# Performance work log

Measured on AMD Instinct MI355X. Metric: run time of the kernel, lower is better.

Reference implementation:

```python
import jax, jax.numpy as jnp
import numpy as np

HEADS = 8
SR = 2
EPS_BN = 1e-5
EPS_LN = 1e-5


def _conv(x, w, b, stride=1, pad=0):
    y = jax.lax.conv_general_dilated(x, w, (stride, stride), [(pad, pad), (pad, pad)],
                                     dimension_numbers=('NCHW', 'OIHW', 'NCHW'))
    return y + b[None, :, None, None]


def _bn(x, g, b):
    # eval-mode BatchNorm with running_mean=0, running_var=1
    return x * (g / jnp.sqrt(1.0 + EPS_BN))[None, :, None, None] + b[None, :, None, None]


def _dwt_haar(x):
    # [B,c,H,W] -> [B,4c,H/2,W/2] stacked as LL,HL,LH,HH (Wave-ViT convention)
    x1 = x[:, :, 0::2, 0::2] / 2
    x2 = x[:, :, 1::2, 0::2] / 2
    x3 = x[:, :, 0::2, 1::2] / 2
    x4 = x[:, :, 1::2, 1::2] / 2
    ll = x1 + x2 + x3 + x4
    hl = -x1 - x2 + x3 + x4
    lh = -x1 + x2 - x3 + x4
    hh = x1 - x2 - x3 + x4
    return jnp.concatenate([ll, hl, lh, hh], axis=1)


def _idwt_haar(y):
    # [B,4c,h,w] -> [B,c,2h,2w], exact inverse of _dwt_haar
    c = y.shape[1] // 4
    ll, hl, lh, hh = y[:, :c], y[:, c:2 * c], y[:, 2 * c:3 * c], y[:, 3 * c:]
    p1 = (ll - hl - lh + hh) / 2  # (0::2, 0::2)
    p2 = (ll - hl + lh - hh) / 2  # (1::2, 0::2)
    p3 = (ll + hl - lh - hh) / 2  # (0::2, 1::2)
    p4 = (ll + hl + lh + hh) / 2  # (1::2, 1::2)
    B, _, h2, w2 = ll.shape
    row0 = jnp.stack([p1, p3], axis=-1)  # even rows
    row1 = jnp.stack([p2, p4], axis=-1)  # odd rows
    out = jnp.stack([row0, row1], axis=3)  # [B,c,h2,2,w2,2]
    return out.reshape(B, c, 2 * h2, 2 * w2)


def setup_inputs() -> dict:
    key = jax.random.key(0)
    ks = jax.random.split(key, 12)
    B, H, W, C = 8, 56, 56, 512
    N = H * W
    c4 = C // 4

    def nrm(k, shp, std):
        return jax.random.normal(k, shp, jnp.float32) * std

    return {
        'x': jax.random.normal(ks[0], (B, N, C), jnp.float32),
        'H': H, 'W': W,
        'reduce_w': nrm(ks[1], (c4, C, 1, 1), (2.0 / c4) ** 0.5),
        'reduce_b': jnp.zeros((c4,), jnp.float32),
        'reduce_g': jnp.ones((c4,), jnp.float32),
        'reduce_beta': jnp.zeros((c4,), jnp.float32),
        'filter_w': nrm(ks[2], (C, C, 3, 3), (2.0 / (9 * C)) ** 0.5),
        'filter_b': jnp.zeros((C,), jnp.float32),
        'filter_g': jnp.ones((C,), jnp.float32),
        'filter_beta': jnp.zeros((C,), jnp.float32),
        'q_w': nrm(ks[3], (C, C), 0.02),
        'q_b': jnp.zeros((C,), jnp.float32),
        'ln_g': jnp.ones((C,), jnp.float32),
        'ln_b': jnp.zeros((C,), jnp.float32),
        'kv_w': nrm(ks[4], (2 * C, C), 0.02),
        'kv_b': jnp.zeros((2 * C,), jnp.float32),
        'kve_w': nrm(ks[5], (C, C, SR, SR), (2.0 / (SR * SR * C)) ** 0.5),
        'kve_b': jnp.zeros((C,), jnp.float32),
        'proj_w': nrm(ks[6], (C, C + c4), 0.02),
        'proj_b': jnp.zeros((C,), jnp.float32),
    }


def reference(x, H, W, reduce_w, reduce_b, reduce_g, reduce_beta,
              filter_w, filter_b, filter_g, filter_beta,
              q_w, q_b, ln_g, ln_b, kv_w, kv_b, kve_w, kve_b, proj_w, proj_b):
    B, N, C = x.shape
    hd = C // HEADS
    scale = hd ** -0.5

    q = (x @ q_w.T + q_b).reshape(B, N, HEADS, hd).transpose(0, 2, 1, 3)  # [B,h,N,d]

    xi = x.reshape(B, H, W, C).transpose(0, 3, 1, 2)  # NCHW
    r = jax.nn.relu(_bn(_conv(xi, reduce_w, reduce_b), reduce_g, reduce_beta))  # [B,C/4,H,W]
    r16 = r.astype(jnp.float16)
    x_dwt = _dwt_haar(r16).astype(jnp.float32)  # [B,C,H/2,W/2]
    x_dwt = jax.nn.relu(_bn(_conv(x_dwt, filter_w, filter_b, pad=1), filter_g, filter_beta))
    x_dwt16 = x_dwt.astype(jnp.float16)
    x_idwt = _idwt_haar(x_dwt16)  # [B,C/4,H,W] fp16
    x_idwt = x_idwt.reshape(B, C // 4, H * W).transpose(0, 2, 1)  # [B,N,C/4]

    x_dwt = x_dwt16.astype(jnp.float32)
    kv_in = _conv(x_dwt, kve_w, kve_b, stride=SR).reshape(B, C, -1).transpose(0, 2, 1)  # [B,M,C]
    mu = kv_in.mean(-1, keepdims=True)
    var = ((kv_in - mu) ** 2).mean(-1, keepdims=True)
    kv_n = (kv_in - mu) / jnp.sqrt(var + EPS_LN) * ln_g + ln_b
    kv = (kv_n @ kv_w.T + kv_b).reshape(B, -1, 2, HEADS, hd).transpose(2, 0, 3, 1, 4)
    k, v = kv[0], kv[1]  # [B,h,M,d]

    attn = jax.nn.softmax(jnp.einsum('bhnd,bhmd->bhnm', q, k) * scale, axis=-1)
    o = jnp.einsum('bhnm,bhmd->bhnd', attn, v).transpose(0, 2, 1, 3).reshape(B, N, C)
    o = jnp.concatenate([o, x_idwt.astype(jnp.float32)], axis=-1)  # [B,N,C+C/4]
    return o @ proj_w.T + proj_b
```

## Files before the change

kernel.cpp:

```cpp
#include <hip/hip_runtime.h>
#include <math.h>


typedef _Float16 half8 __attribute__((ext_vector_type(8)));
typedef _Float16 half4v __attribute__((ext_vector_type(4)));
typedef float f32x4 __attribute__((ext_vector_type(4)));

static const size_t OFF_X16  = 0;
static const size_t OFF_Q16  = 12845056;
static const size_t OFF_CAT  = 25690112;
static const size_t OFF_R16  = 41746432;
static const size_t OFF_PAD  = 44957696;
static const size_t OFF_DWTB = 48644096;
static const size_t OFF_KVIN = 51855360;
static const size_t OFF_LN16 = 55066624;
static const size_t OFF_KV16 = 55869440;
static const size_t OFF_WT   = 57475072;
static const size_t OFF_KT   = 59834368;
static const size_t OFF_QW   = 60882944;
static const size_t OFF_KVW  = 61145088;
static const size_t OFF_PW   = 61669376;
static const size_t OFF_RW   = 61997056;
static const size_t OFF_VT   = 62062592;
static const size_t OFF_PART = 62980096;

#define BN_RSQ 0.9999950000374997f
#define SCL2   0.1803368801111204f
#define PART_STRIDE 3211264
#define KVE_STRIDE  802816

__device__ __forceinline__ void async_copy16(const _Float16* g, _Float16* l) {
    __builtin_amdgcn_global_load_lds(
        (const __attribute__((address_space(1))) void*)g,
        (__attribute__((address_space(3))) void*)l, 16, 0, 0);
}

#define WAIT4_BARRIER() asm volatile("s_waitcnt vmcnt(4)\n\ts_barrier" ::: "memory")
#define WAIT0_BARRIER() asm volatile("s_waitcnt vmcnt(0)\n\ts_barrier" ::: "memory")

template <int ALOAD, int EPI>
__global__ __launch_bounds__(256) void gemm16(
    const _Float16* __restrict__ A, const _Float16* __restrict__ W,
    void* __restrict__ outp, int M, int K, int lda, int ldc,
    const float* __restrict__ bias, const float* __restrict__ bng,
    const float* __restrict__ bnb)
{
    __shared__ _Float16 sA[3][128 * 32];
    __shared__ _Float16 sB[3][128 * 32];
    const int t = threadIdx.x;
    const int lane = t & 63, wid = t >> 6;

    int bx = blockIdx.x, by = blockIdx.y;
    {
        int nwg = gridDim.x * gridDim.y;
        if ((nwg & 7) == 0) {
            int orig = by * gridDim.x + bx;
            int cs = nwg >> 3;
            int wg = (orig & 7) * cs + (orig >> 3);
            by = wg % gridDim.y;
            bx = wg / gridDim.y;
        }
    }
    const int m0 = bx * 128, n0 = by * 128;
    const int kbase = blockIdx.z * K;

    const int sr = wid * 16 + (lane >> 2);
    const int sc = (lane & 3) * 8;
    const int stA0 = wid * 512;
    const int stA1 = 2048 + wid * 512;

    const _Float16 *aP0, *aP1;
    if constexpr (ALOAD == 0) {
        int r0 = m0 + sr;      if (r0 > M - 1) r0 = M - 1;
        int r1 = m0 + 64 + sr; if (r1 > M - 1) r1 = M - 1;
        aP0 = A + (size_t)r0 * lda + sc;
        aP1 = A + (size_t)r1 * lda + sc;
    } else {
        int m_ = m0 + sr; if (m_ > M - 1) m_ = M - 1;
        int b_ = m_ / 196, rem = m_ - b_ * 196, i_ = rem / 14, j_ = rem - i_ * 14;
        aP0 = A + ((size_t)(b_ * 784 + 2 * i_ * 28 + 2 * j_)) * 512 + sc;
        m_ = m0 + 64 + sr; if (m_ > M - 1) m_ = M - 1;
        b_ = m_ / 196; rem = m_ - b_ * 196; i_ = rem / 14; j_ = rem - i_ * 14;
        aP1 = A + ((size_t)(b_ * 784 + 2 * i_ * 28 + 2 * j_)) * 512 + sc;
    }
    const int ldw = (ALOAD == 2) ? lda : K;
    const _Float16* bP0 = W + (size_t)(n0 + sr) * ldw + sc;
    const _Float16* bP1 = W + (size_t)(n0 + 64 + sr) * ldw + sc;

    const int mw = wid & 1, nw = wid >> 1;
    const int pAoff = (mw * 64 + (lane & 15)) * 32 + (lane >> 4) * 8;
    const int pBoff = (nw * 64 + (lane & 15)) * 32 + (lane >> 4) * 8;

    f32x4 acc[4][4];
#pragma unroll
    for (int i = 0; i < 4; ++i)
#pragma unroll
        for (int j = 0; j < 4; ++j) acc[i][j] = (f32x4)(0.0f);

    auto aoff_of = [&](int k) -> int {
        if constexpr (ALOAD == 0) {
            return k;
        } else {
            int sub = k >> 9; int ky = sub >> 1, kx = sub & 1;
            return (ky * 28 + kx) * 512 + (k & 511);
        }
    };
    auto stage = [&](int ti, int buf) {
        int k = kbase + ti * 32;
        int aOff = aoff_of(k);
        async_copy16(aP0 + aOff, &sA[buf][stA0]);
        async_copy16(aP1 + aOff, &sA[buf][stA1]);
        async_copy16(bP0 + k, &sB[buf][stA0]);
        async_copy16(bP1 + k, &sB[buf][stA1]);
    };

    const int nt = K >> 5;
    stage(0, 0);
    if (nt > 1) { stage(1, 1); WAIT4_BARRIER(); }
    else        { WAIT0_BARRIER(); }

    int cur = 0;
    for (int i = 0; i < nt; ++i) {
        const _Float16* pA = &sA[cur][0] + pAoff;
        const _Float16* pB = &sB[cur][0] + pBoff;
        half8 aF[4], bF[4];
#pragma unroll
        for (int u = 0; u < 4; ++u) aF[u] = *(const half8*)(pA + u * 512);
#pragma unroll
        for (int u = 0; u < 4; ++u) bF[u] = *(const half8*)(pB + u * 512);

        const bool st = (i + 2 < nt);
        if (st) {
            int nb = cur + 2; if (nb >= 3) nb -= 3;
            stage(i + 2, nb);
        }
#pragma unroll
        for (int u = 0; u < 4; ++u)
#pragma unroll
            for (int j = 0; j < 4; ++j)
                acc[u][j] = __builtin_amdgcn_mfma_f32_16x16x32_f16(
                    aF[u], bF[j], acc[u][j], 0, 0, 0);

        if (i + 1 < nt) {
            if (st) WAIT4_BARRIER();
            else    WAIT0_BARRIER();
        }
        ++cur; if (cur == 3) cur = 0;
    }

    const int orow = m0 + mw * 64 + (lane >> 4) * 4;
    const int ocol = n0 + nw * 64 + (lane & 15);
#pragma unroll
    for (int j = 0; j < 4; ++j) {
        int col = ocol + j * 16;
        float bv = 0.0f, g = 0.0f, b2 = 0.0f;
        if constexpr (EPI != 3) bv = bias[col];
        if constexpr (EPI == 1) { g = bng[col] * BN_RSQ; b2 = bnb[col]; }
#pragma unroll
        for (int i = 0; i < 4; ++i) {
#pragma unroll
            for (int r = 0; r < 4; ++r) {
                int row = orow + i * 16 + r;
                if (row >= M) continue;
                float v = acc[i][j][r] + bv;
                if constexpr (EPI == 1) v = fmaxf(v * g + b2, 0.0f);
                if constexpr (EPI == 0)
                    ((float*)outp)[(size_t)row * ldc + col] = v;
                else if constexpr (EPI == 3)
                    ((float*)outp)[(size_t)blockIdx.z * KVE_STRIDE
                                   + (size_t)row * ldc + col] = v;
                else
                    ((_Float16*)outp)[(size_t)row * ldc + col] = (_Float16)v;
            }
        }
    }
}

__global__ __launch_bounds__(256) void conv_splitk(
    const _Float16* __restrict__ A, const _Float16* __restrict__ W,
    float* __restrict__ partA, float* __restrict__ partB)
{
    __shared__ _Float16 sA[3][128 * 32];
    __shared__ _Float16 sB[3][128 * 32];
    const int t = threadIdx.x;
    const int lane = t & 63, wid = t >> 6;

    int orig = blockIdx.x;
    int wg = (orig & 7) * 98 + (orig >> 3);
    int bx = wg % 49;  int c = wg / 49;
    int by = c & 3,    bz = c >> 2;

    const int m0 = bx * 128, n0 = by * 128;
    const int kbase = bz * 1152;

    const int sr = wid * 16 + (lane >> 2);
    const int sc = (lane & 3) * 8;
    const int stA0 = wid * 512;
    const int stA1 = 2048 + wid * 512;

    int m_ = m0 + sr;
    int b_ = m_ / 784, rem = m_ - b_ * 784, y_ = rem / 28, x_ = rem - y_ * 28;
    const _Float16* aP0 = A + ((size_t)(b_ * 900 + (y_ + 1) * 30 + (x_ + 1))) * 512 + sc;
    m_ = m0 + 64 + sr;
    b_ = m_ / 784; rem = m_ - b_ * 784; y_ = rem / 28; x_ = rem - y_ * 28;
    const _Float16* aP1 = A + ((size_t)(b_ * 900 + (y_ + 1) * 30 + (x_ + 1))) * 512 + sc;
    const _Float16* bP0 = W + (size_t)(n0 + sr) * 4608 + sc;
    const _Float16* bP1 = W + (size_t)(n0 + 64 + sr) * 4608 + sc;

    const int mw = wid & 1, nw = wid >> 1;
    const int pAoff = (mw * 64 + (lane & 15)) * 32 + (lane >> 4) * 8;
    const int pBoff = (nw * 64 + (lane & 15)) * 32 + (lane >> 4) * 8;

    f32x4 acc[4][4];
#pragma unroll
    for (int i = 0; i < 4; ++i)
#pragma unroll
        for (int j = 0; j < 4; ++j) acc[i][j] = (f32x4)(0.0f);

    auto aoff_of = [&](int k) -> int {
        int sub = k >> 9; int s3 = sub / 3;
        int dy = s3 - 1, dx = sub - s3 * 3 - 1;
        return (dy * 30 + dx) * 512 + (k & 511);
    };
    auto stage = [&](int ti, int buf) {
        int k = kbase + ti * 32;
        int aOff = aoff_of(k);
        async_copy16(aP0 + aOff, &sA[buf][stA0]);
        async_copy16(aP1 + aOff, &sA[buf][stA1]);
        async_copy16(bP0 + k, &sB[buf][stA0]);
        async_copy16(bP1 + k, &sB[buf][stA1]);
    };

    const int nt = 36;
    stage(0, 0);
    stage(1, 1);
    WAIT4_BARRIER();

    int cur = 0;
    for (int i = 0; i < nt; ++i) {
        const _Float16* pA = &sA[cur][0] + pAoff;
        const _Float16* pB = &sB[cur][0] + pBoff;
        half8 aF[4], bF[4];
#pragma unroll
        for (int u = 0; u < 4; ++u) aF[u] = *(const half8*)(pA + u * 512);
#pragma unroll
        for (int u = 0; u < 4; ++u) bF[u] = *(const half8*)(pB + u * 512);

        const bool st = (i + 2 < nt);
        if (st) {
            int nb = cur + 2; if (nb >= 3) nb -= 3;
            stage(i + 2, nb);
        }
#pragma unroll
        for (int u = 0; u < 4; ++u)
#pragma unroll
            for (int j = 0; j < 4; ++j)
                acc[u][j] = __builtin_amdgcn_mfma_f32_16x16x32_f16(
                    aF[u], bF[j], acc[u][j], 0, 0, 0);

        if (i + 1 < nt) {
            if (st) WAIT4_BARRIER();
            else    WAIT0_BARRIER();
        }
        ++cur; if (cur == 3) cur = 0;
    }

    float* dst = (bz < 2) ? (partA + (size_t)bz * PART_STRIDE)
                          : (partB + (size_t)(bz - 2) * PART_STRIDE);
    const int orow = m0 + mw * 64 + (lane >> 4) * 4;
    const int ocol = n0 + nw * 64 + (lane & 15);
#pragma unroll
    for (int j = 0; j < 4; ++j) {
#pragma unroll
        for (int i = 0; i < 4; ++i)
#pragma unroll
            for (int r = 0; r < 4; ++r)
                dst[(size_t)(orow + i * 16 + r) * 512 + ocol + j * 16] = acc[i][j][r];
    }
}

__global__ __launch_bounds__(256) void conv_epi(
    const float* __restrict__ pA, const float* __restrict__ pB,
    _Float16* __restrict__ o, const float* __restrict__ bias,
    const float* __restrict__ bng, const float* __restrict__ bnb)
{
    int i = blockIdx.x * 256 + threadIdx.x;
    size_t base = (size_t)i * 8;
    int c = (int)(base & 511);
    half8 hv;
#pragma unroll
    for (int u = 0; u < 8; u += 4) {
        float4 a0 = *(const float4*)(pA + base + u);
        float4 a1 = *(const float4*)(pA + PART_STRIDE + base + u);
        float4 a2 = *(const float4*)(pB + base + u);
        float4 a3 = *(const float4*)(pB + PART_STRIDE + base + u);
        float s[4] = {a0.x + a1.x + a2.x + a3.x, a0.y + a1.y + a2.y + a3.y,
                      a0.z + a1.z + a2.z + a3.z, a0.w + a1.w + a2.w + a3.w};
#pragma unroll
        for (int v = 0; v < 4; ++v) {
            int cc = c + u + v;
            float val = (s[v] + bias[cc]) * (bng[cc] * BN_RSQ) + bnb[cc];
            hv[u + v] = (_Float16)fmaxf(val, 0.0f);
        }
    }
    *(half8*)(o + base) = hv;
}

__global__ __launch_bounds__(256) void cvt_f32_f16(
    const float* __restrict__ s, _Float16* __restrict__ d, int n8)
{
    int i = blockIdx.x * 256 + threadIdx.x;
    if (i >= n8) return;
    const float4* sp = (const float4*)(s + (size_t)i * 8);
    float4 a = sp[0], b = sp[1];
    half8 h;
    h[0] = (_Float16)a.x; h[1] = (_Float16)a.y; h[2] = (_Float16)a.z; h[3] = (_Float16)a.w;
    h[4] = (_Float16)b.x; h[5] = (_Float16)b.y; h[6] = (_Float16)b.z; h[7] = (_Float16)b.w;
    *(half8*)(d + (size_t)i * 8) = h;
}

__global__ __launch_bounds__(256) void zero_half(_Float16* __restrict__ p, int n8)
{
    int i = blockIdx.x * 256 + threadIdx.x;
    if (i < n8) *(float4*)(p + (size_t)i * 8) = make_float4(0.f, 0.f, 0.f, 0.f);
}

__global__ __launch_bounds__(256) void transpose_filter16(
    const float* __restrict__ fw, _Float16* __restrict__ wT)
{
    int idx = blockIdx.x * 256 + threadIdx.x;
    int n = idx / 4608; int r = idx - n * 4608;
    int sub = r >> 9; int ci = r & 511;
    wT[idx] = (_Float16)fw[(size_t)n * 4608 + ci * 9 + sub];
}

__global__ __launch_bounds__(256) void transpose_kve16(
    const float* __restrict__ kw, _Float16* __restrict__ kT)
{
    int idx = blockIdx.x * 256 + threadIdx.x;
    int n = idx >> 11; int r = idx & 2047;
    int sub = r >> 9; int ci = r & 511;
    kT[idx] = (_Float16)kw[((size_t)n << 11) + (ci << 2) + sub];
}

__global__ __launch_bounds__(256) void vt_prep(
    const _Float16* __restrict__ kv, _Float16* __restrict__ vt)
{
    int idx = blockIdx.x * 256 + threadIdx.x;
    int m = idx % 224;
    int rest = idx / 224;
    int d = rest & 63;
    int bh = rest >> 6;
    int b = bh >> 3, h = bh & 7;
    _Float16 v = (_Float16)0.0f;
    if (m < 196)
        v = kv[((size_t)(b * 196 + m)) * 1024 + 512 + h * 64 + d];
    vt[idx] = v;
}

__global__ __launch_bounds__(128) void dwt_kernel(
    const _Float16* __restrict__ r, _Float16* __restrict__ pad)
{
    int bid = blockIdx.x;
    int b = bid / 784; int rem = bid - b * 784;
    int i = rem / 28;  int j = rem - i * 28;
    int c = threadIdx.x;
    int y = 2 * i, x = 2 * j;
    size_t base = (size_t)b * 3136;
    _Float16 f1 = r[(base + (size_t)y * 56 + x) * 128 + c];
    _Float16 f2 = r[(base + (size_t)(y + 1) * 56 + x) * 128 + c];
    _Float16 f3 = r[(base + (size_t)y * 56 + (x + 1)) * 128 + c];
    _Float16 f4 = r[(base + (size_t)(y + 1) * 56 + (x + 1)) * 128 + c];
    _Float16 h = (_Float16)0.5f;
    _Float16 x1 = f1 * h, x2 = f2 * h, x3 = f3 * h, x4 = f4 * h;
    _Float16 ll = ((x1 + x2) + x3) + x4;
    _Float16 hl = (((-x1) - x2) + x3) + x4;
    _Float16 lh = (((-x1) + x2) - x3) + x4;
    _Float16 hh = ((x1 - x2) - x3) + x4;
    size_t ob = ((size_t)b * 900 + (size_t)(i + 1) * 30 + (j + 1)) * 512;
    pad[ob + c]       = ll;
    pad[ob + 128 + c] = hl;
    pad[ob + 256 + c] = lh;
    pad[ob + 384 + c] = hh;
}

__global__ __launch_bounds__(128) void idwt_kernel(
    const _Float16* __restrict__ d, _Float16* __restrict__ cat)
{
    int bid = blockIdx.x;
    int b = bid / 784; int rem = bid - b * 784;
    int i = rem / 28;  int j = rem - i * 28;
    int c = threadIdx.x;
    size_t ib = ((size_t)b * 784 + (size_t)i * 28 + j) * 512;
    _Float16 ll = d[ib + c];
    _Float16 hl = d[ib + 128 + c];
    _Float16 lh = d[ib + 256 + c];
    _Float16 hh = d[ib + 384 + c];
    _Float16 h = (_Float16)0.5f;
    _Float16 p1 = (((ll - hl) - lh) + hh) * h;
    _Float16 p2 = (((ll - hl) + lh) - hh) * h;
    _Float16 p3 = (((ll + hl) - lh) - hh) * h;
    _Float16 p4 = (((ll + hl) + lh) + hh) * h;
    int y = 2 * i, x = 2 * j;
    size_t rb = (size_t)b * 3136;
    cat[(rb + (size_t)y * 56 + x) * 640 + 512 + c]           = p1;
    cat[(rb + (size_t)y * 56 + x + 1) * 640 + 512 + c]       = p3;
    cat[(rb + (size_t)(y + 1) * 56 + x) * 640 + 512 + c]     = p2;
    cat[(rb + (size_t)(y + 1) * 56 + x + 1) * 640 + 512 + c] = p4;
}

__global__ __launch_bounds__(256) void ln_kernel(
    const float* __restrict__ part, _Float16* __restrict__ o,
    const float* __restrict__ g, const float* __restrict__ bta,
    const float* __restrict__ kvb)
{
    int wave = threadIdx.x >> 6;
    int lane = threadIdx.x & 63;
    int row = blockIdx.x * 4 + wave;
    int c = lane * 8;
    const float* rp = part + (size_t)row * 512 + c;
    float v[8];
#pragma unroll
    for (int i = 0; i < 8; i += 4) {
        float4 a0 = *(const float4*)(rp + i);
        float4 a1 = *(const float4*)(rp + KVE_STRIDE + i);
        float4 a2 = *(const float4*)(rp + 2 * KVE_STRIDE + i);
        float4 a3 = *(const float4*)(rp + 3 * KVE_STRIDE + i);
        v[i + 0] = (a0.x + a1.x) + (a2.x + a3.x) + kvb[c + i + 0];
        v[i + 1] = (a0.y + a1.y) + (a2.y + a3.y) + kvb[c + i + 1];
        v[i + 2] = (a0.z + a1.z) + (a2.z + a3.z) + kvb[c + i + 2];
        v[i + 3] = (a0.w + a1.w) + (a2.w + a3.w) + kvb[c + i + 3];
    }
    float s = ((v[0] + v[1]) + (v[2] + v[3])) + ((v[4] + v[5]) + (v[6] + v[7]));
#pragma unroll
    for (int off = 32; off; off >>= 1) s += __shfl_xor(s, off);
    float mu = s * (1.0f / 512.0f);
    float sq = 0.0f;
#pragma unroll
    for (int i = 0; i < 8; ++i) { v[i] -= mu; sq += v[i] * v[i]; }
#pragma unroll
    for (int off = 32; off; off >>= 1) sq += __shfl_xor(sq, off);
    float inv = 1.0f / sqrtf(sq * (1.0f / 512.0f) + 1e-5f);
    half8 hv;
#pragma unroll
    for (int i = 0; i < 8; ++i) hv[i] = (_Float16)(v[i] * inv * g[c + i] + bta[c + i]);
    *(half8*)(o + (size_t)row * 512 + c) = hv;
}

__global__ __launch_bounds__(256) void attn_mfma(
    const _Float16* __restrict__ q, const _Float16* __restrict__ kv,
    const _Float16* __restrict__ vt, _Float16* __restrict__ cat)
{
    __shared__ _Float16 sK[64][72];
    __shared__ _Float16 sVT[64][72];
    __shared__ _Float16 sP[4][16][40];
    int bid = blockIdx.x;
    int qt = bid % 49;
    int h  = (bid / 49) & 7;
    int b  = bid / 392;
    int n0 = qt * 64;
    int t = threadIdx.x, lane = t & 63, wid = t >> 6;
    int quad = lane >> 4, l16 = lane & 15;

    const _Float16* qp = q + ((size_t)(b * 3136 + n0 + wid * 16 + l16)) * 512
                           + h * 64 + quad * 8;
    half8 aQ0 = *(const half8*)qp;
    half8 aQ1 = *(const half8*)(qp + 32);

    f32x4 oacc[4];
#pragma unroll
    for (int i = 0; i < 4; ++i) oacc[i] = (f32x4)(0.0f);
    float lsum[4] = {0.f, 0.f, 0.f, 0.f};

    const _Float16* vtb = vt + ((size_t)((b * 8 + h) * 64)) * 224;

    for (int c0 = 0; c0 < 224; c0 += 64) {
        __syncthreads();
#pragma unroll
        for (int it = 0; it < 2; ++it) {
            int slot = t + 256 * it;
            int row = slot >> 3, c8 = (slot & 7) * 8;
            int m = c0 + row; if (m > 195) m = 195;
            *(half8*)&sK[row][c8] =
                *(const half8*)(kv + ((size_t)(b * 196 + m)) * 1024 + h * 64 + c8);
        }
#pragma unroll
        for (int it = 0; it < 2; ++it) {
            int slot = t + 256 * it;
            int row = slot >> 3, c8 = (slot & 7) * 8;
            *(half8*)&sVT[row][c8] =
                *(const half8*)(vtb + (size_t)row * 224 + c0 + c8);
        }
        __syncthreads();

#pragma unroll
        for (int sc = 0; sc < 64; sc += 32) {
            half8 bk00 = *(const half8*)&sK[sc + l16][quad * 8];
            half8 bk01 = *(const half8*)&sK[sc + l16][32 + quad * 8];
            half8 bk10 = *(const half8*)&sK[sc + 16 + l16][quad * 8];
            half8 bk11 = *(const half8*)&sK[sc + 16 + l16][32 + quad * 8];
            f32x4 s0 = (f32x4)(0.0f), s1 = (f32x4)(0.0f);
            s0 = __builtin_amdgcn_mfma_f32_16x16x32_f16(aQ0, bk00, s0, 0, 0, 0);
            s0 = __builtin_amdgcn_mfma_f32_16x16x32_f16(aQ1, bk01, s0, 0, 0, 0);
            s1 = __builtin_amdgcn_mfma_f32_16x16x32_f16(aQ0, bk10, s1, 0, 0, 0);
            s1 = __builtin_amdgcn_mfma_f32_16x16x32_f16(aQ1, bk11, s1, 0, 0, 0);

            int col0 = c0 + sc + l16;
            float msk0 = (col0 < 196) ? 0.0f : -INFINITY;
            float msk1 = (col0 + 16 < 196) ? 0.0f : -INFINITY;
            float p0[4], p1[4];
#pragma unroll
            for (int r = 0; r < 4; ++r) {
                p0[r] = exp2f(s0[r] * SCL2 + msk0);
                p1[r] = exp2f(s1[r] * SCL2 + msk1);
                lsum[r] += p0[r] + p1[r];
            }
#pragma unroll
            for (int r = 0; r < 4; ++r) {
                sP[wid][quad * 4 + r][l16]      = (_Float16)p0[r];
                sP[wid][quad * 4 + r][16 + l16] = (_Float16)p1[r];
            }
            half8 aP = *(const half8*)&sP[wid][l16][quad * 8];
            half8 bv0 = *(const half8*)&sVT[l16][sc + quad * 8];
            half8 bv1 = *(const half8*)&sVT[16 + l16][sc + quad * 8];
            half8 bv2 = *(const half8*)&sVT[32 + l16][sc + quad * 8];
            half8 bv3 = *(const half8*)&sVT[48 + l16][sc + quad * 8];
            oacc[0] = __builtin_amdgcn_mfma_f32_16x16x32_f16(aP, bv0, oacc[0], 0, 0, 0);
            oacc[1] = __builtin_amdgcn_mfma_f32_16x16x32_f16(aP, bv1, oacc[1], 0, 0, 0);
            oacc[2] = __builtin_amdgcn_mfma_f32_16x16x32_f16(aP, bv2, oacc[2], 0, 0, 0);
            oacc[3] = __builtin_amdgcn_mfma_f32_16x16x32_f16(aP, bv3, oacc[3], 0, 0, 0);
        }
    }

    float inv[4];
#pragma unroll
    for (int r = 0; r < 4; ++r) {
        float s = lsum[r];
        s += __shfl_xor(s, 1);
        s += __shfl_xor(s, 2);
        s += __shfl_xor(s, 4);
        s += __shfl_xor(s, 8);
        inv[r] = 1.0f / s;
    }
#pragma unroll
    for (int r = 0; r < 4; ++r) {
        size_t rowoff = ((size_t)(b * 3136 + n0 + wid * 16 + quad * 4 + r)) * 640
                        + h * 64 + l16;
#pragma unroll
        for (int tv = 0; tv < 4; ++tv)
            cat[rowoff + tv * 16] = (_Float16)(oacc[tv][r] * inv[r]);
    }
}

extern "C" void kernel_launch(void* const* d_in, const int* in_sizes, int n_in,
                              void* d_out, int out_size, void* d_ws, size_t ws_size,
                              hipStream_t stream)
{
    const float* x           = (const float*)d_in[0];
    const float* reduce_w    = (const float*)d_in[3];
    const float* reduce_b    = (const float*)d_in[4];
    const float* reduce_g    = (const float*)d_in[5];
    const float* reduce_beta = (const float*)d_in[6];
    const float* filter_w    = (const float*)d_in[7];
    const float* filter_b    = (const float*)d_in[8];
    const float* filter_g    = (const float*)d_in[9];
    const float* filter_beta = (const float*)d_in[10];
    const float* q_w         = (const float*)d_in[11];
    const float* q_b         = (const float*)d_in[12];
    const float* ln_g        = (const float*)d_in[13];
    const float* ln_b        = (const float*)d_in[14];
    const float* kv_w        = (const float*)d_in[15];
    const float* kv_b        = (const float*)d_in[16];
    const float* kve_w       = (const float*)d_in[17];
    const float* kve_b       = (const float*)d_in[18];
    const float* proj_w      = (const float*)d_in[19];
    const float* proj_b      = (const float*)d_in[20];
    float* out = (float*)d_out;
    _Float16* hws = (_Float16*)d_ws;

    _Float16* x16    = hws + OFF_X16;
    _Float16* q16    = hws + OFF_Q16;
    _Float16* cat16  = hws + OFF_CAT;
    _Float16* r16    = hws + OFF_R16;
    _Float16* pad16  = hws + OFF_PAD;
    _Float16* dwtb16 = hws + OFF_DWTB;
    _Float16* ln16   = hws + OFF_LN16;
    _Float16* kv16   = hws + OFF_KV16;
    _Float16* wT16   = hws + OFF_WT;
    _Float16* kT16   = hws + OFF_KT;
    _Float16* qw16   = hws + OFF_QW;
    _Float16* kvw16  = hws + OFF_KVW;
    _Float16* pw16   = hws + OFF_PW;
    _Float16* rw16   = hws + OFF_RW;
    _Float16* vt16   = hws + OFF_VT;
    float*    partA  = (float*)(hws + OFF_X16);
    float*    partB  = (float*)(hws + OFF_PART);
    float*    kvepart = (float*)(hws + OFF_X16);

    cvt_f32_f16<<<dim3(6272), dim3(256), 0, stream>>>(x, x16, 1605632);
    cvt_f32_f16<<<dim3(128),  dim3(256), 0, stream>>>(q_w, qw16, 32768);
    cvt_f32_f16<<<dim3(256),  dim3(256), 0, stream>>>(kv_w, kvw16, 65536);
    cvt_f32_f16<<<dim3(160),  dim3(256), 0, stream>>>(proj_w, pw16, 40960);
    cvt_f32_f16<<<dim3(32),   dim3(256), 0, stream>>>(reduce_w, rw16, 8192);
    transpose_filter16<<<dim3(9216), dim3(256), 0, stream>>>(filter_w, wT16);
    transpose_kve16<<<dim3(4096), dim3(256), 0, stream>>>(kve_w, kT16);
    zero_half<<<dim3(1800), dim3(256), 0, stream>>>(pad16, 460800);

    gemm16<0, 2><<<dim3(196, 4), dim3(256), 0, stream>>>(
        x16, qw16, q16, 25088, 512, 512, 512, q_b, nullptr, nullptr);

    gemm16<0, 1><<<dim3(196, 1), dim3(256), 0, stream>>>(
        x16, rw16, r16, 25088, 512, 512, 128, reduce_b, reduce_g, reduce_beta);

    dwt_kernel<<<dim3(6272), dim3(128), 0, stream>>>(r16, pad16);

    conv_splitk<<<dim3(784), dim3(256), 0, stream>>>(pad16, wT16, partA, partB);
    conv_epi<<<dim3(1568), dim3(256), 0, stream>>>(
        partA, partB, dwtb16, filter_b, filter_g, filter_beta);

    idwt_kernel<<<dim3(6272), dim3(128), 0, stream>>>(dwtb16, cat16);

    gemm16<2, 3><<<dim3(13, 4, 4), dim3(256), 0, stream>>>(
        dwtb16, kT16, kvepart, 1568, 512, 2048, 512, nullptr, nullptr, nullptr);

    ln_kernel<<<dim3(392), dim3(256), 0, stream>>>(kvepart, ln16, ln_g, ln_b, kve_b);

    gemm16<0, 2><<<dim3(13, 8), dim3(256), 0, stream>>>(
        ln16, kvw16, kv16, 1568, 512, 512, 1024, kv_b, nullptr, nullptr);

    vt_prep<<<dim3(3584), dim3(256), 0, stream>>>(kv16, vt16);

    attn_mfma<<<dim3(3136), dim3(256), 0, stream>>>(q16, kv16, vt16, cat16);

    gemm16<0, 0><<<dim3(196, 4), dim3(256), 0, stream>>>(
        cat16, pw16, out, 25088, 640, 640, 512, proj_b, nullptr, nullptr);
}
```

Baseline: 421.5 us.

## Fuse q and reduce GEMMs into one launch and use nontemporal stores

The q projection and the 1x1 reduce conv both read x16, so their weights are now concatenated into one buffer and computed by a single GEMM launch with 5 column tiles. A new epilogue mode routes the last tile through bias+BN+ReLU into r16 and the others into q16. Separately, streaming outputs (fp32 GEMM outputs, split-K partials, cat writes) use nontemporal stores, and conv_epi reads its partials with nontemporal loads, to reduce cache pollution. This saves one launch and one pass over x16, at the cost of a per-tile branch in the epilogue.

```diff
diff --git a/kernel.cpp b/kernel.cpp
--- a/kernel.cpp
+++ b/kernel.cpp
@@ -12,7 +12,7 @@
 static const size_t OFF_R16  = 41746432;
 static const size_t OFF_PAD  = 44957696;
 static const size_t OFF_DWTB = 48644096;
-static const size_t OFF_KVIN = 51855360;
+static const size_t OFF_QRW  = 51855360;
 static const size_t OFF_LN16 = 55066624;
 static const size_t OFF_KV16 = 55869440;
 static const size_t OFF_WT   = 57475072;
@@ -43,7 +43,8 @@
     const _Float16* __restrict__ A, const _Float16* __restrict__ W,
     void* __restrict__ outp, int M, int K, int lda, int ldc,
     const float* __restrict__ bias, const float* __restrict__ bng,
-    const float* __restrict__ bnb)
+    const float* __restrict__ bnb, const float* __restrict__ bias2,
+    void* __restrict__ outp2)
 {
     __shared__ _Float16 sA[3][128 * 32];
     __shared__ _Float16 sB[3][128 * 32];
@@ -154,7 +155,17 @@
     for (int j = 0; j < 4; ++j) {
         int col = ocol + j * 16;
         float bv = 0.0f, g = 0.0f, b2 = 0.0f;
-        if constexpr (EPI != 3) bv = bias[col];
+        if constexpr (EPI == 4) {
+            if (n0 >= 512) {
+                bv = bias2[col - 512];
+                g = bng[col - 512] * BN_RSQ;
+                b2 = bnb[col - 512];
+            } else {
+                bv = bias[col];
+            }
+        } else if constexpr (EPI != 3) {
+            bv = bias[col];
+        }
         if constexpr (EPI == 1) { g = bng[col] * BN_RSQ; b2 = bnb[col]; }
 #pragma unroll
         for (int i = 0; i < 4; ++i) {
@@ -164,13 +175,24 @@
                 if (row >= M) continue;
                 float v = acc[i][j][r] + bv;
                 if constexpr (EPI == 1) v = fmaxf(v * g + b2, 0.0f);
-                if constexpr (EPI == 0)
-                    ((float*)outp)[(size_t)row * ldc + col] = v;
-                else if constexpr (EPI == 3)
-                    ((float*)outp)[(size_t)blockIdx.z * KVE_STRIDE
-                                   + (size_t)row * ldc + col] = v;
-                else
+                if constexpr (EPI == 0) {
+                    __builtin_nontemporal_store(
+                        v, (float*)outp + (size_t)row * ldc + col);
+                } else if constexpr (EPI == 3) {
+                    __builtin_nontemporal_store(
+                        v, (float*)outp + (size_t)blockIdx.z * KVE_STRIDE
+                           + (size_t)row * ldc + col);
+                } else if constexpr (EPI == 4) {
+                    if (n0 >= 512) {
+                        v = fmaxf(v * g + b2, 0.0f);
+                        ((_Float16*)outp2)[(size_t)row * 128 + (col - 512)] =
+                            (_Float16)v;
+                    } else {
+                        ((_Float16*)outp)[(size_t)row * ldc + col] = (_Float16)v;
+                    }
+                } else {
                     ((_Float16*)outp)[(size_t)row * ldc + col] = (_Float16)v;
+                }
             }
         }
     }
@@ -275,7 +297,9 @@
         for (int i = 0; i < 4; ++i)
 #pragma unroll
             for (int r = 0; r < 4; ++r)
-                dst[(size_t)(orow + i * 16 + r) * 512 + ocol + j * 16] = acc[i][j][r];
+                __builtin_nontemporal_store(
+                    acc[i][j][r],
+                    &dst[(size_t)(orow + i * 16 + r) * 512 + ocol + j * 16]);
     }
 }
 
@@ -290,16 +314,15 @@
     half8 hv;
 #pragma unroll
     for (int u = 0; u < 8; u += 4) {
-        float4 a0 = *(const float4*)(pA + base + u);
-        float4 a1 = *(const float4*)(pA + PART_STRIDE + base + u);
-        float4 a2 = *(const float4*)(pB + base + u);
-        float4 a3 = *(const float4*)(pB + PART_STRIDE + base + u);
-        float s[4] = {a0.x + a1.x + a2.x + a3.x, a0.y + a1.y + a2.y + a3.y,
-                      a0.z + a1.z + a2.z + a3.z, a0.w + a1.w + a2.w + a3.w};
+        f32x4 a0 = __builtin_nontemporal_load((const f32x4*)(pA + base + u));
+        f32x4 a1 = __builtin_nontemporal_load((const f32x4*)(pA + PART_STRIDE + base + u));
+        f32x4 a2 = __builtin_nontemporal_load((const f32x4*)(pB + base + u));
+        f32x4 a3 = __builtin_nontemporal_load((const f32x4*)(pB + PART_STRIDE + base + u));
 #pragma unroll
         for (int v = 0; v < 4; ++v) {
             int cc = c + u + v;
-            float val = (s[v] + bias[cc]) * (bng[cc] * BN_RSQ) + bnb[cc];
+            float s = (a0[v] + a1[v]) + (a2[v] + a3[v]);
+            float val = (s + bias[cc]) * (bng[cc] * BN_RSQ) + bnb[cc];
             hv[u + v] = (_Float16)fmaxf(val, 0.0f);
         }
     }
@@ -403,10 +426,10 @@
     _Float16 p4 = (((ll + hl) + lh) + hh) * h;
     int y = 2 * i, x = 2 * j;
     size_t rb = (size_t)b * 3136;
-    cat[(rb + (size_t)y * 56 + x) * 640 + 512 + c]           = p1;
-    cat[(rb + (size_t)y * 56 + x + 1) * 640 + 512 + c]       = p3;
-    cat[(rb + (size_t)(y + 1) * 56 + x) * 640 + 512 + c]     = p2;
-    cat[(rb + (size_t)(y + 1) * 56 + x + 1) * 640 + 512 + c] = p4;
+    __builtin_nontemporal_store(p1, &cat[(rb + (size_t)y * 56 + x) * 640 + 512 + c]);
+    __builtin_nontemporal_store(p3, &cat[(rb + (size_t)y * 56 + x + 1) * 640 + 512 + c]);
+    __builtin_nontemporal_store(p2, &cat[(rb + (size_t)(y + 1) * 56 + x) * 640 + 512 + c]);
+    __builtin_nontemporal_store(p4, &cat[(rb + (size_t)(y + 1) * 56 + x + 1) * 640 + 512 + c]);
 }
 
 __global__ __launch_bounds__(256) void ln_kernel(
@@ -548,7 +571,8 @@
                         + h * 64 + l16;
 #pragma unroll
         for (int tv = 0; tv < 4; ++tv)
-            cat[rowoff + tv * 16] = (_Float16)(oacc[tv][r] * inv[r]);
+            __builtin_nontemporal_store(
+                (_Float16)(oacc[tv][r] * inv[r]), &cat[rowoff + tv * 16]);
     }
 }
 
@@ -584,33 +608,30 @@
     _Float16* r16    = hws + OFF_R16;
     _Float16* pad16  = hws + OFF_PAD;
     _Float16* dwtb16 = hws + OFF_DWTB;
+    _Float16* qrw16  = hws + OFF_QRW;
     _Float16* ln16   = hws + OFF_LN16;
     _Float16* kv16   = hws + OFF_KV16;
     _Float16* wT16   = hws + OFF_WT;
     _Float16* kT16   = hws + OFF_KT;
-    _Float16* qw16   = hws + OFF_QW;
     _Float16* kvw16  = hws + OFF_KVW;
     _Float16* pw16   = hws + OFF_PW;
-    _Float16* rw16   = hws + OFF_RW;
     _Float16* vt16   = hws + OFF_VT;
     float*    partA  = (float*)(hws + OFF_X16);
     float*    partB  = (float*)(hws + OFF_PART);
     float*    kvepart = (float*)(hws + OFF_X16);
 
     cvt_f32_f16<<<dim3(6272), dim3(256), 0, stream>>>(x, x16, 1605632);
-    cvt_f32_f16<<<dim3(128),  dim3(256), 0, stream>>>(q_w, qw16, 32768);
+    cvt_f32_f16<<<dim3(128),  dim3(256), 0, stream>>>(q_w, qrw16, 32768);
+    cvt_f32_f16<<<dim3(32),   dim3(256), 0, stream>>>(reduce_w, qrw16 + 262144, 8192);
     cvt_f32_f16<<<dim3(256),  dim3(256), 0, stream>>>(kv_w, kvw16, 65536);
     cvt_f32_f16<<<dim3(160),  dim3(256), 0, stream>>>(proj_w, pw16, 40960);
-    cvt_f32_f16<<<dim3(32),   dim3(256), 0, stream>>>(reduce_w, rw16, 8192);
     transpose_filter16<<<dim3(9216), dim3(256), 0, stream>>>(filter_w, wT16);
     transpose_kve16<<<dim3(4096), dim3(256), 0, stream>>>(kve_w, kT16);
     zero_half<<<dim3(1800), dim3(256), 0, stream>>>(pad16, 460800);
 
-    gemm16<0, 2><<<dim3(196, 4), dim3(256), 0, stream>>>(
-        x16, qw16, q16, 25088, 512, 512, 512, q_b, nullptr, nullptr);
-
-    gemm16<0, 1><<<dim3(196, 1), dim3(256), 0, stream>>>(
-        x16, rw16, r16, 25088, 512, 512, 128, reduce_b, reduce_g, reduce_beta);
+    gemm16<0, 4><<<dim3(196, 5), dim3(256), 0, stream>>>(
+        x16, qrw16, q16, 25088, 512, 512, 512, q_b, reduce_g, reduce_beta,
+        reduce_b, r16);
 
     dwt_kernel<<<dim3(6272), dim3(128), 0, stream>>>(r16, pad16);
 
@@ -621,17 +642,20 @@
     idwt_kernel<<<dim3(6272), dim3(128), 0, stream>>>(dwtb16, cat16);
 
     gemm16<2, 3><<<dim3(13, 4, 4), dim3(256), 0, stream>>>(
-        dwtb16, kT16, kvepart, 1568, 512, 2048, 512, nullptr, nullptr, nullptr);
+        dwtb16, kT16, kvepart, 1568, 512, 2048, 512, nullptr, nullptr, nullptr,
+        nullptr, nullptr);
 
     ln_kernel<<<dim3(392), dim3(256), 0, stream>>>(kvepart, ln16, ln_g, ln_b, kve_b);
 
     gemm16<0, 2><<<dim3(13, 8), dim3(256), 0, stream>>>(
-        ln16, kvw16, kv16, 1568, 512, 512, 1024, kv_b, nullptr, nullptr);
+        ln16, kvw16, kv16, 1568, 512, 512, 1024, kv_b, nullptr, nullptr,
+        nullptr, nullptr);
 
     vt_prep<<<dim3(3584), dim3(256), 0, stream>>>(kv16, vt16);
 
     attn_mfma<<<dim3(3136), dim3(256), 0, stream>>>(q16, kv16, vt16, cat16);
 
     gemm16<0, 0><<<dim3(196, 4), dim3(256), 0, stream>>>(
-        cat16, pw16, out, 25088, 640, 640, 512, proj_b, nullptr, nullptr);
-}
+        cat16, pw16, out, 25088, 640, 640, 512, proj_b, nullptr, nullptr,
+        nullptr, nullptr);
+}
```

Measured after the change: 411.2 us. 1.03x faster.
